# Performance work log

Measured on AMD Instinct MI355X. Metric: run time of the kernel, lower is better.

Reference implementation:

```python
import jax, jax.numpy as jnp
import numpy as np
import math

D = 1024  # output_dim (power of 2)
IN = 1024  # input dim
CAP = int(math.log2(D))  # number of butterfly stages


def _gen_indices(s):
    """Static FFT-butterfly index lists (numpy, computed at trace time)."""
    def ind_s(k):
        if k == 0:
            return [np.array([1, 0])]
        temp = np.arange(2 ** k)
        list0 = [np.concatenate([temp + 2 ** k, temp])]
        list1 = ind_s(k - 1)
        for i in range(k):
            list0.append(np.concatenate([list1[i], list1[i] + 2 ** k]))
        return list0

    t = ind_s(int(math.log2(s // 2)))
    cap = int(math.log2(s))
    ind_exe = [np.asarray(t[i], dtype=np.int32) for i in range(cap)]
    ind_param = []
    for i in range(cap):
        ind = np.concatenate([np.arange(0, s, 2 ** i) + j for j in range(2 ** i)]).astype(np.int32)
        ind_param.append(ind)
    return ind_exe, ind_param


IND_EXE, IND_PARAM = _gen_indices(D)


def setup_inputs() -> dict:
    key = jax.random.key(0)
    ks = jax.random.split(key, 9)
    B = 8192
    x = jax.random.normal(ks[0], (B, IN), dtype=jnp.float32)
    state = jax.random.normal(ks[1], (B, D), dtype=jnp.float32)
    theta = jax.random.uniform(ks[2], (CAP, D // 2), minval=-3.14, maxval=3.14, dtype=jnp.float32)
    U = jax.random.uniform(ks[3], (IN, 3 * D), minval=-0.01, maxval=0.01, dtype=jnp.float32)
    W_r = jax.random.uniform(ks[4], (D, D), minval=-0.01, maxval=0.01, dtype=jnp.float32)
    W_g = jax.random.uniform(ks[5], (D, D), minval=-0.01, maxval=0.01, dtype=jnp.float32)
    bias_r = jnp.full((D,), 2.0, dtype=jnp.float32)
    bias_g = jnp.zeros((D,), dtype=jnp.float32)
    bias_c = jnp.full((D,), 0.01, dtype=jnp.float32)
    return {"x": x, "state": state, "theta": theta, "U": U, "W_r": W_r,
            "W_g": W_g, "bias_r": bias_r, "bias_g": bias_g, "bias_c": bias_c}


def reference(x, state, theta, U, W_r, W_g, bias_r, bias_g, bias_c):
    # fft_param: rotation coefficients, permuted by the static ind_param lists
    cos_list = jnp.concatenate([jnp.cos(theta), jnp.cos(theta)], axis=1)   # [CAP, D]
    sin_list = jnp.concatenate([jnp.sin(theta), -jnp.sin(theta)], axis=1)  # [CAP, D]
    v1 = jnp.stack([cos_list[i][IND_PARAM[i]] for i in range(CAP)])  # [CAP, D]
    v2 = jnp.stack([sin_list[i][IND_PARAM[i]] for i in range(CAP)])  # [CAP, D]

    Ux = x @ U                                   # [B, 3D]
    U_cx, U_rx, U_gx = jnp.split(Ux, 3, axis=1)  # each [B, D]
    r = jax.nn.sigmoid(U_rx + state @ W_r + bias_r)
    g = jax.nn.sigmoid(U_gx + state @ W_g + bias_g)

    # butterfly orthogonal rotation of the state
    h = state
    for i in range(CAP):
        h = h * v1[i] + (h * v2[i])[:, IND_EXE[i]]

    # modReLU
    pre = r * h + U_cx
    c = jnp.sign(pre) * jax.nn.relu(jnp.abs(pre) + 0.001 + bias_c)

    out = g * state + (1.0 - g) * c
    return out
```

## Files before the change

kernel.cpp:

```cpp
#include <hip/hip_runtime.h>
#include <hip/hip_bf16.h>
#include <stdint.h>


typedef __bf16 bf16x8 __attribute__((ext_vector_type(8)));
typedef float f32x4 __attribute__((ext_vector_type(4)));

#define B_ROWS 8192
#define KDIM 1024

__device__ __forceinline__ void async16(__bf16* lds, const __hip_bfloat16* g) {
    __builtin_amdgcn_global_load_lds((const __attribute__((address_space(1))) void*)g,
                                     (__attribute__((address_space(3))) void*)lds,
                                     16, 0, 0);
}

__global__ __launch_bounds__(256) void cast_kernel(const float* __restrict__ src,
                                                   __hip_bfloat16* __restrict__ dst) {
    int idx = blockIdx.x * 256 + threadIdx.x;
    const float4 v = ((const float4*)src)[idx];
    __hip_bfloat16* d = dst + (size_t)idx * 4;
    d[0] = __float2bfloat16(v.x);
    d[1] = __float2bfloat16(v.y);
    d[2] = __float2bfloat16(v.z);
    d[3] = __float2bfloat16(v.w);
}

__global__ __launch_bounds__(256) void transpose_cast(const float* __restrict__ src,
                                                      __hip_bfloat16* __restrict__ dst,
                                                      int N, int rowOff) {
    __shared__ float tile[32][33];
    int n0 = blockIdx.x * 32;
    int k0 = blockIdx.y * 32;
    int tx = threadIdx.x & 31;
    int ty = threadIdx.x >> 5;
#pragma unroll
    for (int s = 0; s < 4; ++s) {
        int k = k0 + ty + s * 8;
        tile[ty + s * 8][tx] = src[(size_t)k * N + n0 + tx];
    }
    __syncthreads();
#pragma unroll
    for (int s = 0; s < 4; ++s) {
        int n = n0 + ty + s * 8;
        dst[(size_t)(rowOff + n) * KDIM + k0 + tx] = __float2bfloat16(tile[tx][ty + s * 8]);
    }
}

__global__ __launch_bounds__(256) void table_kernel(const float* __restrict__ theta,
                                                    float* __restrict__ v1,
                                                    float* __restrict__ v2) {
    int idx = blockIdx.x * 256 + threadIdx.x;
    int i = idx >> 10;
    int j = idx & 1023;
    int Q = 1024 >> i;
    int j0 = j / Q;
    int m = j & (Q - 1);
    int q = (m << i) + j0;
    float th = theta[i * 512 + (q & 511)];
    float c = cosf(th);
    float s = sinf(th);
    v1[idx] = c;
    v2[idx] = (q < 512) ? s : -s;
}

__global__ __launch_bounds__(256) void gemm_fused(const __hip_bfloat16* __restrict__ xb,
                                                  const __hip_bfloat16* __restrict__ sb,
                                                  const __hip_bfloat16* __restrict__ Wt,
                                                  const float* __restrict__ bias_r,
                                                  const float* __restrict__ bias_g,
                                                  __hip_bfloat16* __restrict__ P) {
    __shared__ __align__(16) __bf16 As[128 * 32];
    __shared__ __align__(16) __bf16 Bs[128 * 32];

    const int nt = blockIdx.x;
    const int mt = blockIdx.y;
    const int group = nt >> 3;
    const int c0 = (nt & 7) * 128;
    const int mBase = mt * 128;

    const int t = threadIdx.x;
    const int lane = t & 63;
    const int wv = t >> 6;
    const int wm = wv & 1;
    const int wn = wv >> 1;
    const int r0 = lane & 15;
    const int gq = lane >> 4;

    f32x4 acc[4][4];
    const f32x4 zero = {0.f, 0.f, 0.f, 0.f};
#pragma unroll
    for (int i = 0; i < 4; ++i)
#pragma unroll
        for (int j = 0; j < 4; ++j) acc[i][j] = zero;

    const int rowA0 = t >> 2;
    const int sub = (t & 3) * 8;

    const int nphase = (group == 0) ? 1 : 2;
    for (int ph = 0; ph < nphase; ++ph) {
        const __hip_bfloat16* Ab = ph ? sb : xb;
        int bRow;
        if (group == 0)      bRow = c0;
        else if (group == 1) bRow = ph ? (3072 + c0) : (1024 + c0);
        else                 bRow = ph ? (4096 + c0) : (2048 + c0);
        const __hip_bfloat16* Bb = Wt + (size_t)bRow * KDIM;

        for (int k0 = 0; k0 < KDIM; k0 += 32) {
#pragma unroll
            for (int p = 0; p < 2; ++p) {
                int chunk = p * 256 + t;
                int row = p * 64 + rowA0;
                async16(&As[chunk * 8], Ab + (size_t)(mBase + row) * KDIM + k0 + sub);
                async16(&Bs[chunk * 8], Bb + (size_t)row * KDIM + k0 + sub);
            }
            __syncthreads();

            bf16x8 af[4], bf[4];
#pragma unroll
            for (int i = 0; i < 4; ++i)
                af[i] = *reinterpret_cast<const bf16x8*>(&As[(wm * 64 + i * 16 + r0) * 32 + gq * 8]);
#pragma unroll
            for (int j = 0; j < 4; ++j)
                bf[j] = *reinterpret_cast<const bf16x8*>(&Bs[(wn * 64 + j * 16 + r0) * 32 + gq * 8]);
#pragma unroll
            for (int i = 0; i < 4; ++i)
#pragma unroll
                for (int j = 0; j < 4; ++j)
                    acc[i][j] = __builtin_amdgcn_mfma_f32_16x16x32_bf16(af[i], bf[j], acc[i][j], 0, 0, 0);
            __syncthreads();
        }
    }

#pragma unroll
    for (int i = 0; i < 4; ++i) {
#pragma unroll
        for (int j = 0; j < 4; ++j) {
#pragma unroll
            for (int reg = 0; reg < 4; ++reg) {
                int row = mBase + wm * 64 + i * 16 + gq * 4 + reg;
                int cl = wn * 64 + j * 16 + r0;
                float v = acc[i][j][reg];
                int colG;
                if (group == 0) {
                    colG = c0 + cl;
                } else {
                    int c = c0 + cl;
                    float b = (group == 1) ? bias_r[c] : bias_g[c];
                    v = 1.0f / (1.0f + __expf(-(v + b)));
                    colG = ((group == 1) ? 1024 : 2048) + c;
                }
                P[(size_t)row * 3072 + colG] = __float2bfloat16(v);
            }
        }
    }
}

__global__ __launch_bounds__(256) void fuse_kernel(const float* __restrict__ state,
                                                   const __hip_bfloat16* __restrict__ P,
                                                   const float* __restrict__ v1,
                                                   const float* __restrict__ v2,
                                                   const float* __restrict__ bias_c,
                                                   float* __restrict__ out) {
    __shared__ float hbuf[8][1024];
    const int t = threadIdx.x;
    const int rowBase = blockIdx.x * 8;

    float sreg[8][4];
#pragma unroll
    for (int r = 0; r < 8; ++r) {
#pragma unroll
        for (int e = 0; e < 4; ++e) {
            int col = t + 256 * e;
            float s = state[(size_t)(rowBase + r) * 1024 + col];
            hbuf[r][col] = s;
            sreg[r][e] = s;
        }
    }
    __syncthreads();

    for (int i = 0; i < 10; ++i) {
        int H = 512 >> i;
        float t1[4], t2[4];
#pragma unroll
        for (int e = 0; e < 4; ++e) {
            int j = t + 256 * e;
            t1[e] = v1[i * 1024 + j];
            t2[e] = v2[i * 1024 + (j ^ H)];
        }
        float nh[8][4];
#pragma unroll
        for (int r = 0; r < 8; ++r)
#pragma unroll
            for (int e = 0; e < 4; ++e) {
                int j = t + 256 * e;
                nh[r][e] = hbuf[r][j] * t1[e] + hbuf[r][j ^ H] * t2[e];
            }
        __syncthreads();
#pragma unroll
        for (int r = 0; r < 8; ++r)
#pragma unroll
            for (int e = 0; e < 4; ++e) hbuf[r][t + 256 * e] = nh[r][e];
        __syncthreads();
    }

#pragma unroll
    for (int r = 0; r < 8; ++r) {
#pragma unroll
        for (int e = 0; e < 4; ++e) {
            int col = t + 256 * e;
            int row = rowBase + r;
            float h = hbuf[r][col];
            const size_t pb = (size_t)row * 3072;
            float Ucx = __bfloat162float(P[pb + col]);
            float rr  = __bfloat162float(P[pb + 1024 + col]);
            float gg  = __bfloat162float(P[pb + 2048 + col]);
            float pre = rr * h + Ucx;
            float mag = fabsf(pre) + 0.001f + bias_c[col];
            float c = (pre > 0.f) ? mag : ((pre < 0.f) ? -mag : 0.f);
            out[(size_t)row * 1024 + col] = gg * sreg[r][e] + (1.f - gg) * c;
        }
    }
}

extern "C" void kernel_launch(void* const* d_in, const int* in_sizes, int n_in,
                              void* d_out, int out_size, void* d_ws, size_t ws_size,
                              hipStream_t stream) {
    const float* x      = (const float*)d_in[0];
    const float* state  = (const float*)d_in[1];
    const float* theta  = (const float*)d_in[2];
    const float* U      = (const float*)d_in[3];
    const float* W_r    = (const float*)d_in[4];
    const float* W_g    = (const float*)d_in[5];
    const float* bias_r = (const float*)d_in[6];
    const float* bias_g = (const float*)d_in[7];
    const float* bias_c = (const float*)d_in[8];
    float* out = (float*)d_out;

    __hip_bfloat16* xb = (__hip_bfloat16*)d_ws;
    __hip_bfloat16* sb = xb + (size_t)B_ROWS * KDIM;
    __hip_bfloat16* Wt = sb + (size_t)B_ROWS * KDIM;
    __hip_bfloat16* P  = Wt + (size_t)5120 * KDIM;
    float* v1 = (float*)(P + (size_t)B_ROWS * 3072);
    float* v2 = v1 + 10 * 1024;

    cast_kernel<<<8192, 256, 0, stream>>>(x, xb);
    cast_kernel<<<8192, 256, 0, stream>>>(state, sb);
    transpose_cast<<<dim3(96, 32), 256, 0, stream>>>(U,   Wt, 3072, 0);
    transpose_cast<<<dim3(32, 32), 256, 0, stream>>>(W_r, Wt, 1024, 3072);
    transpose_cast<<<dim3(32, 32), 256, 0, stream>>>(W_g, Wt, 1024, 4096);
    table_kernel<<<40, 256, 0, stream>>>(theta, v1, v2);
    gemm_fused<<<dim3(24, 64), 256, 0, stream>>>(xb, sb, Wt, bias_r, bias_g, P);
    fuse_kernel<<<1024, 256, 0, stream>>>(state, P, v1, v2, bias_c, out);
}
```

Baseline: 303.3 us.

## Concatenate x/state and weights along K, swizzle LDS, widen K-tile, vectorize epilogue

Result: slower. 322.3 us (+6.2%).

```diff
diff --git a/kernel.cpp b/kernel.cpp
--- a/kernel.cpp
+++ b/kernel.cpp
@@ -4,10 +4,10 @@
 
 
 typedef __bf16 bf16x8 __attribute__((ext_vector_type(8)));
+typedef __bf16 bf16x4 __attribute__((ext_vector_type(4)));
 typedef float f32x4 __attribute__((ext_vector_type(4)));
 
 #define B_ROWS 8192
-#define KDIM 1024
 
 __device__ __forceinline__ void async16(__bf16* lds, const __hip_bfloat16* g) {
     __builtin_amdgcn_global_load_lds((const __attribute__((address_space(1))) void*)g,
@@ -15,36 +15,51 @@
                                      16, 0, 0);
 }
 
-__global__ __launch_bounds__(256) void cast_kernel(const float* __restrict__ src,
-                                                   __hip_bfloat16* __restrict__ dst) {
-    int idx = blockIdx.x * 256 + threadIdx.x;
-    const float4 v = ((const float4*)src)[idx];
-    __hip_bfloat16* d = dst + (size_t)idx * 4;
-    d[0] = __float2bfloat16(v.x);
-    d[1] = __float2bfloat16(v.y);
-    d[2] = __float2bfloat16(v.z);
-    d[3] = __float2bfloat16(v.w);
-}
-
-__global__ __launch_bounds__(256) void transpose_cast(const float* __restrict__ src,
-                                                      __hip_bfloat16* __restrict__ dst,
-                                                      int N, int rowOff) {
+__global__ __launch_bounds__(256) void prep_xs(const float* __restrict__ x,
+                                               const float* __restrict__ state,
+                                               __hip_bfloat16* __restrict__ xs) {
+    const int row = blockIdx.x;
+    const int col = threadIdx.x * 8;
+    const float* src = (col < 1024) ? (x + (size_t)row * 1024 + col)
+                                    : (state + (size_t)row * 1024 + (col - 1024));
+    float4 a = *(const float4*)src;
+    float4 b = *(const float4*)(src + 4);
+    bf16x8 v;
+    v[0] = (__bf16)a.x; v[1] = (__bf16)a.y; v[2] = (__bf16)a.z; v[3] = (__bf16)a.w;
+    v[4] = (__bf16)b.x; v[5] = (__bf16)b.y; v[6] = (__bf16)b.z; v[7] = (__bf16)b.w;
+    *(bf16x8*)((__bf16*)xs + (size_t)row * 2048 + col) = v;
+}
+
+__global__ __launch_bounds__(256) void prep_w(const float* __restrict__ U,
+                                              const float* __restrict__ Wr,
+                                              const float* __restrict__ Wg,
+                                              __hip_bfloat16* __restrict__ Wt0,
+                                              __hip_bfloat16* __restrict__ Wt12) {
     __shared__ float tile[32][33];
-    int n0 = blockIdx.x * 32;
-    int k0 = blockIdx.y * 32;
-    int tx = threadIdx.x & 31;
-    int ty = threadIdx.x >> 5;
-#pragma unroll
-    for (int s = 0; s < 4; ++s) {
-        int k = k0 + ty + s * 8;
-        tile[ty + s * 8][tx] = src[(size_t)k * N + n0 + tx];
-    }
+    const int id = blockIdx.x;
+    const float* src; int srcN, scol, sk;
+    __hip_bfloat16* dst; int dstStride, dn, dk;
+    if (id < 1024) {
+        int nx = id & 31, ky = id >> 5;
+        src = U; srcN = 3072; scol = nx * 32; sk = ky * 32;
+        dst = Wt0; dstStride = 1024; dn = nx * 32; dk = ky * 32;
+    } else {
+        int id2 = id - 1024;
+        int nx = id2 & 63, ky = id2 >> 6;
+        int n0 = nx * 32, k0 = ky * 32;
+        dst = Wt12; dstStride = 2048; dn = n0; dk = k0;
+        if (k0 < 1024)      { src = U;  srcN = 3072; scol = 1024 + n0; sk = k0; }
+        else if (n0 < 1024) { src = Wr; srcN = 1024; scol = n0;        sk = k0 - 1024; }
+        else                { src = Wg; srcN = 1024; scol = n0 - 1024; sk = k0 - 1024; }
+    }
+    const int tx = threadIdx.x & 31, ty = threadIdx.x >> 5;
+#pragma unroll
+    for (int s = 0; s < 4; ++s)
+        tile[ty + s * 8][tx] = src[(size_t)(sk + ty + s * 8) * srcN + scol + tx];
     __syncthreads();
 #pragma unroll
-    for (int s = 0; s < 4; ++s) {
-        int n = n0 + ty + s * 8;
-        dst[(size_t)(rowOff + n) * KDIM + k0 + tx] = __float2bfloat16(tile[tx][ty + s * 8]);
-    }
+    for (int s = 0; s < 4; ++s)
+        dst[(size_t)(dn + ty + s * 8) * dstStride + dk + tx] = __float2bfloat16(tile[tx][ty + s * 8]);
 }
 
 __global__ __launch_bounds__(256) void table_kernel(const float* __restrict__ theta,
@@ -64,14 +79,14 @@
     v2[idx] = (q < 512) ? s : -s;
 }
 
-__global__ __launch_bounds__(256) void gemm_fused(const __hip_bfloat16* __restrict__ xb,
-                                                  const __hip_bfloat16* __restrict__ sb,
-                                                  const __hip_bfloat16* __restrict__ Wt,
+__global__ __launch_bounds__(256) void gemm_fused(const __hip_bfloat16* __restrict__ xs,
+                                                  const __hip_bfloat16* __restrict__ Wt0,
+                                                  const __hip_bfloat16* __restrict__ Wt12,
                                                   const float* __restrict__ bias_r,
                                                   const float* __restrict__ bias_g,
                                                   __hip_bfloat16* __restrict__ P) {
-    __shared__ __align__(16) __bf16 As[128 * 32];
-    __shared__ __align__(16) __bf16 Bs[128 * 32];
+    __shared__ __align__(16) __bf16 As[128 * 64];
+    __shared__ __align__(16) __bf16 Bs[128 * 64];
 
     const int nt = blockIdx.x;
     const int mt = blockIdx.y;
@@ -87,6 +102,11 @@
     const int r0 = lane & 15;
     const int gq = lane >> 4;
 
+    const __hip_bfloat16* Bb;
+    int bStride, kEnd;
+    if (group == 0) { Bb = Wt0 + (size_t)c0 * 1024; bStride = 1024; kEnd = 1024; }
+    else            { Bb = Wt12 + (size_t)((group == 2 ? 1024 : 0) + c0) * 2048; bStride = 2048; kEnd = 2048; }
+
     f32x4 acc[4][4];
     const f32x4 zero = {0.f, 0.f, 0.f, 0.f};
 #pragma unroll
@@ -94,42 +114,39 @@
 #pragma unroll
         for (int j = 0; j < 4; ++j) acc[i][j] = zero;
 
-    const int rowA0 = t >> 2;
-    const int sub = (t & 3) * 8;
-
-    const int nphase = (group == 0) ? 1 : 2;
-    for (int ph = 0; ph < nphase; ++ph) {
-        const __hip_bfloat16* Ab = ph ? sb : xb;
-        int bRow;
-        if (group == 0)      bRow = c0;
-        else if (group == 1) bRow = ph ? (3072 + c0) : (1024 + c0);
-        else                 bRow = ph ? (4096 + c0) : (2048 + c0);
-        const __hip_bfloat16* Bb = Wt + (size_t)bRow * KDIM;
-
-        for (int k0 = 0; k0 < KDIM; k0 += 32) {
-#pragma unroll
-            for (int p = 0; p < 2; ++p) {
-                int chunk = p * 256 + t;
-                int row = p * 64 + rowA0;
-                async16(&As[chunk * 8], Ab + (size_t)(mBase + row) * KDIM + k0 + sub);
-                async16(&Bs[chunk * 8], Bb + (size_t)row * KDIM + k0 + sub);
-            }
-            __syncthreads();
-
+    for (int k0 = 0; k0 < kEnd; k0 += 64) {
+#pragma unroll
+        for (int p = 0; p < 4; ++p) {
+            int c = p * 256 + t;
+            int row = c >> 3;
+            int jj = ((c & 7) ^ (row & 7)) * 8;
+            async16(&As[c * 8], xs + (size_t)(mBase + row) * 2048 + k0 + jj);
+            async16(&Bs[c * 8], Bb + (size_t)row * bStride + k0 + jj);
+        }
+        __syncthreads();
+
+#pragma unroll
+        for (int s = 0; s < 2; ++s) {
             bf16x8 af[4], bf[4];
 #pragma unroll
-            for (int i = 0; i < 4; ++i)
-                af[i] = *reinterpret_cast<const bf16x8*>(&As[(wm * 64 + i * 16 + r0) * 32 + gq * 8]);
-#pragma unroll
-            for (int j = 0; j < 4; ++j)
-                bf[j] = *reinterpret_cast<const bf16x8*>(&Bs[(wn * 64 + j * 16 + r0) * 32 + gq * 8]);
+            for (int i = 0; i < 4; ++i) {
+                int row = wm * 64 + i * 16 + r0;
+                int cc = row * 8 + ((s * 4 + gq) ^ (row & 7));
+                af[i] = *reinterpret_cast<const bf16x8*>(&As[cc * 8]);
+            }
+#pragma unroll
+            for (int j = 0; j < 4; ++j) {
+                int row = wn * 64 + j * 16 + r0;
+                int cc = row * 8 + ((s * 4 + gq) ^ (row & 7));
+                bf[j] = *reinterpret_cast<const bf16x8*>(&Bs[cc * 8]);
+            }
 #pragma unroll
             for (int i = 0; i < 4; ++i)
 #pragma unroll
                 for (int j = 0; j < 4; ++j)
                     acc[i][j] = __builtin_amdgcn_mfma_f32_16x16x32_bf16(af[i], bf[j], acc[i][j], 0, 0, 0);
-            __syncthreads();
-        }
+        }
+        __syncthreads();
     }
 
 #pragma unroll
@@ -139,18 +156,17 @@
 #pragma unroll
             for (int reg = 0; reg < 4; ++reg) {
                 int row = mBase + wm * 64 + i * 16 + gq * 4 + reg;
-                int cl = wn * 64 + j * 16 + r0;
+                int c = c0 + wn * 64 + j * 16 + r0;
                 float v = acc[i][j][reg];
-                int colG;
                 if (group == 0) {
-                    colG = c0 + cl;
+                    P[(size_t)row * 3072 + c] = __float2bfloat16(v);
+                } else if (group == 1) {
+                    float z = 1.0f / (1.0f + __expf(-(v + bias_r[c])));
+                    P[(size_t)row * 3072 + 1024 + 2 * c] = __float2bfloat16(z);
                 } else {
-                    int c = c0 + cl;
-                    float b = (group == 1) ? bias_r[c] : bias_g[c];
-                    v = 1.0f / (1.0f + __expf(-(v + b)));
-                    colG = ((group == 1) ? 1024 : 2048) + c;
+                    float z = 1.0f / (1.0f + __expf(-(v + bias_g[c])));
+                    P[(size_t)row * 3072 + 1024 + 2 * c + 1] = __float2bfloat16(z);
                 }
-                P[(size_t)row * 3072 + colG] = __float2bfloat16(v);
             }
         }
     }
@@ -166,16 +182,12 @@
     const int t = threadIdx.x;
     const int rowBase = blockIdx.x * 8;
 
-    float sreg[8][4];
+    float4 sreg[8];
 #pragma unroll
     for (int r = 0; r < 8; ++r) {
-#pragma unroll
-        for (int e = 0; e < 4; ++e) {
-            int col = t + 256 * e;
-            float s = state[(size_t)(rowBase + r) * 1024 + col];
-            hbuf[r][col] = s;
-            sreg[r][e] = s;
-        }
+        float4 s4 = ((const float4*)(state + (size_t)(rowBase + r) * 1024))[t];
+        sreg[r] = s4;
+        *(float4*)&hbuf[r][4 * t] = s4;
     }
     __syncthreads();
 
@@ -204,22 +216,30 @@
         __syncthreads();
     }
 
+    const float4 bc = ((const float4*)bias_c)[t];
+    const float bcv[4] = {bc.x, bc.y, bc.z, bc.w};
 #pragma unroll
     for (int r = 0; r < 8; ++r) {
+        const int row = rowBase + r;
+        const float4 h4 = *(const float4*)&hbuf[r][4 * t];
+        const float hv[4] = {h4.x, h4.y, h4.z, h4.w};
+        const float sv[4] = {sreg[r].x, sreg[r].y, sreg[r].z, sreg[r].w};
+        const __hip_bfloat16* Pr = P + (size_t)row * 3072;
+        bf16x4 ux = *(const bf16x4*)((const __bf16*)Pr + 4 * t);
+        bf16x8 rg = *(const bf16x8*)((const __bf16*)Pr + 1024 + 8 * t);
+        float o[4];
 #pragma unroll
         for (int e = 0; e < 4; ++e) {
-            int col = t + 256 * e;
-            int row = rowBase + r;
-            float h = hbuf[r][col];
-            const size_t pb = (size_t)row * 3072;
-            float Ucx = __bfloat162float(P[pb + col]);
-            float rr  = __bfloat162float(P[pb + 1024 + col]);
-            float gg  = __bfloat162float(P[pb + 2048 + col]);
-            float pre = rr * h + Ucx;
-            float mag = fabsf(pre) + 0.001f + bias_c[col];
+            float Ucx = (float)ux[e];
+            float rr  = (float)rg[2 * e];
+            float gg  = (float)rg[2 * e + 1];
+            float pre = rr * hv[e] + Ucx;
+            float mag = fabsf(pre) + 0.001f + bcv[e];
             float c = (pre > 0.f) ? mag : ((pre < 0.f) ? -mag : 0.f);
-            out[(size_t)row * 1024 + col] = gg * sreg[r][e] + (1.f - gg) * c;
-        }
+            o[e] = gg * sv[e] + (1.f - gg) * c;
+        }
+        float4 o4 = {o[0], o[1], o[2], o[3]};
+        ((float4*)(out + (size_t)row * 1024))[t] = o4;
     }
 }
 
@@ -237,19 +257,16 @@
     const float* bias_c = (const float*)d_in[8];
     float* out = (float*)d_out;
 
-    __hip_bfloat16* xb = (__hip_bfloat16*)d_ws;
-    __hip_bfloat16* sb = xb + (size_t)B_ROWS * KDIM;
-    __hip_bfloat16* Wt = sb + (size_t)B_ROWS * KDIM;
-    __hip_bfloat16* P  = Wt + (size_t)5120 * KDIM;
+    __hip_bfloat16* xs   = (__hip_bfloat16*)d_ws;
+    __hip_bfloat16* Wt0  = xs + (size_t)B_ROWS * 2048;
+    __hip_bfloat16* Wt12 = Wt0 + (size_t)1024 * 1024;
+    __hip_bfloat16* P    = Wt12 + (size_t)2048 * 2048;
     float* v1 = (float*)(P + (size_t)B_ROWS * 3072);
     float* v2 = v1 + 10 * 1024;
 
-    cast_kernel<<<8192, 256, 0, stream>>>(x, xb);
-    cast_kernel<<<8192, 256, 0, stream>>>(state, sb);
-    transpose_cast<<<dim3(96, 32), 256, 0, stream>>>(U,   Wt, 3072, 0);
-    transpose_cast<<<dim3(32, 32), 256, 0, stream>>>(W_r, Wt, 1024, 3072);
-    transpose_cast<<<dim3(32, 32), 256, 0, stream>>>(W_g, Wt, 1024, 4096);
+    prep_xs<<<8192, 256, 0, stream>>>(x, state, xs);
+    prep_w<<<5120, 256, 0, stream>>>(U, W_r, W_g, Wt0, Wt12);
     table_kernel<<<40, 256, 0, stream>>>(theta, v1, v2);
-    gemm_fused<<<dim3(24, 64), 256, 0, stream>>>(xb, sb, Wt, bias_r, bias_g, P);
+    gemm_fused<<<dim3(24, 64), 256, 0, stream>>>(xs, Wt0, Wt12, bias_r, bias_g, P);
     fuse_kernel<<<1024, 256, 0, stream>>>(state, P, v1, v2, bias_c, out);
 }
```
